# Kernel optimization log

Hardware: AMD Instinct MI355X
Metric: run time of the kernel (lower is better)

The kernel has to match this reference:

```python
import jax, jax.numpy as jnp
import numpy as np

B, S, H, DK = 2, 2048, 16, 64
D = H * DK  # d_model = 1024


def setup_inputs() -> dict:
    key = jax.random.key(0)
    ks = jax.random.split(key, 12)
    inp = {
        "queries": jax.random.normal(ks[0], (B, S, D), jnp.float32),
        "keys": jax.random.normal(ks[1], (B, S, D), jnp.float32),
        "values": jax.random.normal(ks[2], (B, S, D), jnp.float32),
        # additive 0/1 mask (1 = masked out), causal upper-triangular
        "mask": jnp.triu(jnp.ones((S, S), jnp.float32), k=1)[None, None, :, :],
        "W_q": jax.random.normal(ks[3], (D, D), jnp.float32) / np.sqrt(D),
        "b_q": jnp.zeros((D,), jnp.float32),
        "W_k": jax.random.normal(ks[4], (D, D), jnp.float32) / np.sqrt(D),
        "b_k": jnp.zeros((D,), jnp.float32),
        "W_v": jax.random.normal(ks[5], (D, D), jnp.float32) / np.sqrt(D),
        "b_v": jnp.zeros((D,), jnp.float32),
        "W_o": jax.random.normal(ks[6], (D, D), jnp.float32) / np.sqrt(D),
        "b_o": jnp.zeros((D,), jnp.float32),
    }
    return inp


def _split_heads(x):
    # (B, S, D) -> (B, H, S, DK)
    return x.reshape(x.shape[0], x.shape[1], H, DK).transpose(0, 2, 1, 3)


def reference(queries, keys, values, mask, W_q, b_q, W_k, b_k, W_v, b_v, W_o, b_o):
    q = _split_heads(queries @ W_q + b_q)  # (B, H, S, DK)
    k = _split_heads(keys @ W_k + b_k)
    v = _split_heads(values @ W_v + b_v)
    scale = 1.0 / jnp.sqrt(jnp.asarray(DK, q.dtype))
    scores = jnp.einsum("bhqd,bhkd->bhqk", q, k) * scale  # (B, H, S, S)
    scores = scores + (-1e9) * mask
    weights = jax.nn.softmax(scores, axis=-1)
    o = jnp.einsum("bhqk,bhkd->bhqd", weights, v)  # (B, H, S, DK)
    o = o.transpose(0, 2, 1, 3).reshape(queries.shape[0], queries.shape[1], D)
    return o @ W_o + b_o
```

## Files before the change

kernel.cpp:

```cpp
#include <hip/hip_runtime.h>
#include <hip/hip_bf16.h>
#include <stdint.h>

typedef unsigned short u16;
typedef __attribute__((ext_vector_type(4))) float f32x4;
typedef __attribute__((ext_vector_type(8))) short bf16x8;
typedef __attribute__((ext_vector_type(4))) short s16x4;

#define B_ 2
#define S_ 2048
#define H_ 16
#define D_ 1024
#define XELEMS (B_*S_*D_)
#define WELEMS (D_*D_)
#define QSCALE 0.18033688f

__device__ __forceinline__ u16 f2bf(float f) {
  union { float f; unsigned u; } v; v.f = f;
  unsigned r = v.u + 0x7fffu + ((v.u >> 16) & 1u);
  return (u16)(r >> 16);
}

__device__ __forceinline__ void async16(const void* g, void* l) {
  __builtin_amdgcn_global_load_lds(
      (const __attribute__((address_space(1))) unsigned int*)g,
      (__attribute__((address_space(3))) unsigned int*)l, 16, 0, 0);
}

#if __has_builtin(__builtin_amdgcn_exp2f)
#define EXP2(x) __builtin_amdgcn_exp2f(x)
#else
#define EXP2(x) exp2f(x)
#endif

__device__ __forceinline__ unsigned cvtpk(float a, float b) {
  unsigned r;
  asm("v_cvt_pk_bf16_f32 %0, %1, %2" : "=v"(r) : "v"(a), "v"(b));
  return r;
}

#if __has_builtin(__builtin_amdgcn_mfma_f32_16x16x16bf16_1k)
#define MFMA16(a, b, c) __builtin_amdgcn_mfma_f32_16x16x16bf16_1k(a, b, c, 0, 0, 0)
#else
__device__ __forceinline__ f32x4 mfma16_(s16x4 a, s16x4 b, f32x4 c) {
  asm("v_mfma_f32_16x16x16_bf16 %0, %1, %2, %0" : "+v"(c) : "v"(a), "v"(b));
  return c;
}
#define MFMA16(a, b, c) mfma16_(a, b, c)
#endif

__global__ __launch_bounds__(256) void prep_k(
    const float* __restrict__ q, const float* __restrict__ k,
    const float* __restrict__ v,
    const float* __restrict__ Wq, const float* __restrict__ Wk,
    const float* __restrict__ Wv, const float* __restrict__ Wo,
    u16* __restrict__ X, u16* __restrict__ WT) {
  const int bid = blockIdx.x;
  if (bid < 4096) {
    __shared__ float tile[32][33];
    const int z = bid >> 10, rem = bid & 1023;
    const float* W = (z == 0) ? Wq : (z == 1) ? Wk : (z == 2) ? Wv : Wo;
    u16* o = WT + z * WELEMS;
    const int r0 = (rem >> 5) << 5, c0 = (rem & 31) << 5;
    const int tx = threadIdx.x & 31, ty = threadIdx.x >> 5;
    #pragma unroll
    for (int rr = ty; rr < 32; rr += 8)
      tile[rr][tx] = W[(r0 + rr) * D_ + c0 + tx];
    __syncthreads();
    #pragma unroll
    for (int rr = ty; rr < 32; rr += 8)
      o[(c0 + rr) * D_ + r0 + tx] = f2bf(tile[tx][rr]);
  } else {
    const int cb = bid - 4096;
    const int ngrp = XELEMS / 8;
    const int total = 3 * ngrp;
    for (int i = cb * 256 + threadIdx.x; i < total; i += 1024 * 256) {
      int which = i / ngrp;
      int off = (i - which * ngrp) * 8;
      const float* src = (which == 0) ? q : (which == 1) ? k : v;
      float4 a = *(const float4*)(src + off);
      float4 b = *(const float4*)(src + off + 4);
      u16 rr[8] = {f2bf(a.x), f2bf(a.y), f2bf(a.z), f2bf(a.w),
                   f2bf(b.x), f2bf(b.y), f2bf(b.z), f2bf(b.w)};
      uint4 pk;
      pk.x = (unsigned)rr[0] | ((unsigned)rr[1] << 16);
      pk.y = (unsigned)rr[2] | ((unsigned)rr[3] << 16);
      pk.z = (unsigned)rr[4] | ((unsigned)rr[5] << 16);
      pk.w = (unsigned)rr[6] | ((unsigned)rr[7] << 16);
      *(uint4*)(X + which * XELEMS + off) = pk;
    }
  }
}

template <int MODE, int DBUF>
__device__ __forceinline__ void gemm_body(const u16* __restrict__ A,
                                          const u16* __restrict__ BT,
                                          const float* __restrict__ bias,
                                          void* __restrict__ outp,
                                          int bm, int bn, float scale) {
  constexpr int SMEM_BYTES = DBUF ? 65536 : ((MODE == 0 || MODE == 2) ? 34816 : 32768);
  __shared__ __align__(16) char smem[SMEM_BYTES];
  const int tid = threadIdx.x;
  const int w = tid >> 6, l = tid & 63;
  const int wr = w >> 1, wc = w & 1;
  const int g = l >> 4, r = l & 15;
  (void)w; (void)l;

  f32x4 acc[4][4];
  #pragma unroll
  for (int i = 0; i < 4; i++)
    #pragma unroll
    for (int j = 0; j < 4; j++) acc[i][j] = (f32x4){0.f, 0.f, 0.f, 0.f};

  int dst[4], aoff[4], boff[4];
  #pragma unroll
  for (int i = 0; i < 4; i++) {
    const int o = i * 4096 + tid * 16;
    dst[i] = o;
    const int row = o >> 7;
    const int cbyte = (o & 127) ^ ((row & 7) << 4);
    aoff[i] = (bm + row) * 1024 + (cbyte >> 1);
    boff[i] = (bn + row) * 1024 + (cbyte >> 1);
  }

  if (DBUF == 0) {
    char* Ab = smem;
    char* Bb = smem + 16384;
    for (int t = 0; t < 16; ++t) {
      const int k0 = t * 64;
      #pragma unroll
      for (int i = 0; i < 4; i++) async16(A + aoff[i] + k0, Ab + dst[i]);
      #pragma unroll
      for (int i = 0; i < 4; i++) async16(BT + boff[i] + k0, Bb + dst[i]);
      __syncthreads();
      bf16x8 af[2][4], bf[2][4];
      #pragma unroll
      for (int kk = 0; kk < 2; kk++)
        #pragma unroll
        for (int mi = 0; mi < 4; mi++) {
          const int rA = wr * 64 + mi * 16 + r;
          af[kk][mi] = *(const bf16x8*)(Ab +
              ((rA * 128 + kk * 64 + g * 16) ^ ((rA & 7) << 4)));
        }
      #pragma unroll
      for (int kk = 0; kk < 2; kk++)
        #pragma unroll
        for (int ni = 0; ni < 4; ni++) {
          const int rB = wc * 64 + ni * 16 + r;
          bf[kk][ni] = *(const bf16x8*)(Bb +
              ((rB * 128 + kk * 64 + g * 16) ^ ((rB & 7) << 4)));
        }
      #pragma unroll
      for (int kk = 0; kk < 2; kk++)
        #pragma unroll
        for (int mi = 0; mi < 4; mi++)
          #pragma unroll
          for (int ni = 0; ni < 4; ni++)
            acc[mi][ni] = __builtin_amdgcn_mfma_f32_16x16x32_bf16(
                af[kk][mi], bf[kk][ni], acc[mi][ni], 0, 0, 0);
      __syncthreads();
    }
  } else {
    #pragma unroll
    for (int i = 0; i < 4; i++) {
      async16(A + aoff[i], smem + dst[i]);
      async16(BT + boff[i], smem + 16384 + dst[i]);
    }
    for (int t = 0; t < 16; ++t) {
      const int buf = t & 1;
      const char* Ab = smem + buf * 32768;
      const char* Bb = Ab + 16384;
      if (t < 15) {
        const int k0 = (t + 1) * 64;
        char* An = smem + (buf ^ 1) * 32768;
        #pragma unroll
        for (int i = 0; i < 4; i++) {
          async16(A + aoff[i] + k0, An + dst[i]);
          async16(BT + boff[i] + k0, An + 16384 + dst[i]);
        }
        asm volatile("s_waitcnt vmcnt(8)" ::: "memory");
      } else {
        asm volatile("s_waitcnt vmcnt(0)" ::: "memory");
      }
      asm volatile("s_barrier" ::: "memory");

      bf16x8 af[2][4], bf[2][4];
      #pragma unroll
      for (int kk = 0; kk < 2; kk++)
        #pragma unroll
        for (int mi = 0; mi < 4; mi++) {
          const int rA = wr * 64 + mi * 16 + r;
          af[kk][mi] = *(const bf16x8*)(Ab +
              ((rA * 128 + kk * 64 + g * 16) ^ ((rA & 7) << 4)));
        }
      #pragma unroll
      for (int kk = 0; kk < 2; kk++)
        #pragma unroll
        for (int ni = 0; ni < 4; ni++) {
          const int rB = wc * 64 + ni * 16 + r;
          bf[kk][ni] = *(const bf16x8*)(Bb +
              ((rB * 128 + kk * 64 + g * 16) ^ ((rB & 7) << 4)));
        }
      __builtin_amdgcn_s_setprio(1);
      #pragma unroll
      for (int kk = 0; kk < 2; kk++)
        #pragma unroll
        for (int mi = 0; mi < 4; mi++)
          #pragma unroll
          for (int ni = 0; ni < 4; ni++)
            acc[mi][ni] = __builtin_amdgcn_mfma_f32_16x16x32_bf16(
                af[kk][mi], bf[kk][ni], acc[mi][ni], 0, 0, 0);
      __builtin_amdgcn_s_setprio(0);
      asm volatile("s_barrier" ::: "memory");
    }
  }

  const int col0 = bn + wc * 64;
  float bc[4];
  #pragma unroll
  for (int ni = 0; ni < 4; ni++) bc[ni] = bias[col0 + ni * 16 + r];

  if (MODE == 0) {
    u16* Ts = (u16*)smem;
    #pragma unroll
    for (int mi = 0; mi < 4; mi++) {
      #pragma unroll
      for (int ni = 0; ni < 4; ni++) {
        const int lcol = wc * 64 + ni * 16 + r;
        #pragma unroll
        for (int i = 0; i < 4; i++) {
          const int lrow = wr * 64 + mi * 16 + g * 4 + i;
          Ts[lrow * 136 + lcol] = f2bf((acc[mi][ni][i] + bc[ni]) * scale);
        }
      }
    }
    __syncthreads();
    u16* out = (u16*)outp;
    const int bb = bm >> 11;
    const int sbase = bm & 2047;
    #pragma unroll
    for (int j = 0; j < 8; j++) {
      const int c = j * 256 + tid;
      const int row = c >> 4, oct = c & 15;
      const int col = bn + oct * 8;
      const int h = col >> 6, dk = col & 63;
      bf16x8 vv = *(const bf16x8*)&Ts[row * 136 + oct * 8];
      *(bf16x8*)&out[(((size_t)((bb << 4) | h) * 2048 + sbase + row) << 6) + dk] = vv;
    }
  } else if (MODE == 2) {
    u16* Ts = (u16*)smem;
    #pragma unroll
    for (int mi = 0; mi < 4; mi++) {
      const int lrow = wr * 64 + mi * 16 + g * 4;
      #pragma unroll
      for (int ni = 0; ni < 4; ni++) {
        const int lcol = wc * 64 + ni * 16 + r;
        u16 p0 = f2bf(acc[mi][ni][0] + bc[ni]);
        u16 p1 = f2bf(acc[mi][ni][1] + bc[ni]);
        u16 p2 = f2bf(acc[mi][ni][2] + bc[ni]);
        u16 p3 = f2bf(acc[mi][ni][3] + bc[ni]);
        uint2 pk;
        pk.x = (unsigned)p0 | ((unsigned)p1 << 16);
        pk.y = (unsigned)p2 | ((unsigned)p3 << 16);
        *(uint2*)&Ts[lcol * 136 + lrow] = pk;
      }
    }
    __syncthreads();
    u16* out = (u16*)outp;
    const int bb = bm >> 11;
    const int sbase = bm & 2047;
    #pragma unroll
    for (int j = 0; j < 8; j++) {
      const int c = (tid >> 6) * 512 + j * 64 + (tid & 63);
      const int dk = c >> 4, sc = c & 15;
      const int col = bn + dk;
      const int h = col >> 6, dkk = col & 63;
      bf16x8 vv = *(const bf16x8*)&Ts[dk * 136 + sc * 8];
      *(bf16x8*)&out[(((size_t)(((bb << 4) | h) * 64 + dkk)) << 11) +
                     sbase + sc * 8] = vv;
    }
  } else {
    float* out = (float*)outp;
    #pragma unroll
    for (int mi = 0; mi < 4; mi++) {
      const int row = bm + wr * 64 + mi * 16 + g * 4;
      #pragma unroll
      for (int ni = 0; ni < 4; ni++) {
        const int col = col0 + ni * 16 + r;
        #pragma unroll
        for (int i = 0; i < 4; i++)
          out[(row + i) * 1024 + col] = acc[mi][ni][i] + bc[ni];
      }
    }
  }
}

__global__ __launch_bounds__(256) void gemm_qkv_k(
    const u16* __restrict__ X, const u16* __restrict__ WT,
    const float* __restrict__ bq, const float* __restrict__ bk,
    const float* __restrict__ bv, u16* __restrict__ QKV) {
  const int z = blockIdx.z;
  const float* bias = (z == 0) ? bq : (z == 1) ? bk : bv;
  if (z == 2)
    gemm_body<2, 0>(X + z * XELEMS, WT + z * WELEMS, bias, QKV + z * XELEMS,
                    blockIdx.x * 128, blockIdx.y * 128, 1.0f);
  else
    gemm_body<0, 0>(X + z * XELEMS, WT + z * WELEMS, bias, QKV + z * XELEMS,
                    blockIdx.x * 128, blockIdx.y * 128,
                    (z == 0) ? QSCALE : 1.0f);
}

__global__ __launch_bounds__(256) void gemm_o_k(
    const u16* __restrict__ O, const u16* __restrict__ WOT,
    const float* __restrict__ bo, float* __restrict__ out) {
  gemm_body<1, 1>(O, WOT, bo, out, blockIdx.x * 128, blockIdx.y * 128, 1.0f);
}

__global__ __launch_bounds__(512) void attn_k(
    const u16* __restrict__ Qh, const u16* __restrict__ Kh,
    const u16* __restrict__ VTh, u16* __restrict__ O) {
  __shared__ __align__(16) char ldsK[3][8192];
  __shared__ __align__(16) char ldsV[3][8192];

  const int bh = blockIdx.y;
  const int pj = blockIdx.x;
  const int tid = threadIdx.x;
  const int w = tid >> 6, l = tid & 63;
  const int grp = w >> 2, wg = w & 3;
  const int g = l >> 4, r = l & 15;
  const int b = bh >> 4, h = bh & 15;
  const int pjx = b ? (15 - pj) : pj;

  const u16* Qp = Qh + bh * (S_ * 64);
  const char* Kp = (const char*)(Kh + bh * (S_ * 64));
  const char* Vp = (const char*)(VTh + bh * (64 * S_));

  const int o = w * 1024 + l * 16;
  const int kdst = o;
  const int ksrc = o ^ (((o >> 7) & 7) << 4);
  const int vd = o >> 7, vcb = o & 127;
  const int vfix = vd * (S_ * 2) + (vcb ^ ((vd & 7) << 4));

  const int qt = grp ? (31 - pjx) : pjx;
  const int q0w = qt * 64 + wg * 16;
  const int my_nt = qt + 1;
  const int nt_max = 32 - pjx;
  const int qloc = wg * 16 + r;

  bf16x8 qf[2];
  #pragma unroll
  for (int dh = 0; dh < 2; dh++)
    qf[dh] = *(const bf16x8*)(Qp + (q0w + r) * 64 + dh * 32 + g * 8);
  asm volatile("s_waitcnt vmcnt(0)" ::: "memory");

  f32x4 accT[4];
  #pragma unroll
  for (int dn = 0; dn < 4; dn++) accT[dn] = (f32x4){0.f, 0.f, 0.f, 0.f};
  float mrun = -1e30f, lsum = 0.f;

  async16(Kp + ksrc, &ldsK[0][0] + kdst);
  async16(Vp + vfix, &ldsV[0][0] + kdst);
  async16(Kp + 8192 + ksrc, &ldsK[1][0] + kdst);
  async16(Vp + 128 + vfix, &ldsV[1][0] + kdst);

  int cur = 0, pre = 2;
  for (int t = 0; t < nt_max; ++t) {
    if (t + 2 < nt_max) {
      async16(Kp + (t + 2) * 8192 + ksrc, &ldsK[pre][0] + kdst);
      async16(Vp + (t + 2) * 128 + vfix, &ldsV[pre][0] + kdst);
      asm volatile("s_waitcnt vmcnt(4)" ::: "memory");
    } else if (t + 1 < nt_max) {
      asm volatile("s_waitcnt vmcnt(2)" ::: "memory");
    } else {
      asm volatile("s_waitcnt vmcnt(0)" ::: "memory");
    }
    asm volatile("s_barrier" ::: "memory");

    if (t < my_nt) {
      const char* Kb = &ldsK[cur][0];
      f32x4 sc[4];
      #pragma unroll
      for (int ct = 0; ct < 4; ct++) {
        const int row = ct * 16 + r;
        const int sw = (row & 7) << 4;
        bf16x8 k0 = *(const bf16x8*)(Kb + ((row * 128 + g * 16) ^ sw));
        bf16x8 k1 = *(const bf16x8*)(Kb + ((row * 128 + 64 + g * 16) ^ sw));
        f32x4 z = (f32x4){0.f, 0.f, 0.f, 0.f};
        z = __builtin_amdgcn_mfma_f32_16x16x32_bf16(k0, qf[0], z, 0, 0, 0);
        sc[ct] = __builtin_amdgcn_mfma_f32_16x16x32_bf16(k1, qf[1], z, 0, 0, 0);
      }

      if (t == my_nt - 1) {
        #pragma unroll
        for (int ct = 0; ct < 4; ct++)
          #pragma unroll
          for (int i = 0; i < 4; i++)
            if (ct * 16 + g * 4 + i > qloc) sc[ct][i] = -1e9f;
      }

      float a0 = fmaxf(fmaxf(sc[0][0], sc[0][1]), sc[0][2]);
      float a1 = fmaxf(fmaxf(sc[0][3], sc[1][0]), sc[1][1]);
      float a2 = fmaxf(fmaxf(sc[1][2], sc[1][3]), sc[2][0]);
      float a3 = fmaxf(fmaxf(sc[2][1], sc[2][2]), sc[2][3]);
      float a4 = fmaxf(fmaxf(sc[3][0], sc[3][1]), sc[3][2]);
      float pmax = fmaxf(fmaxf(fmaxf(a0, a1), fmaxf(a2, a3)),
                         fmaxf(a4, sc[3][3]));

      if (!__all(pmax - mrun <= 11.0f)) {
        float pm = fmaxf(pmax, __shfl_xor(pmax, 16, 64));
        pm = fmaxf(pm, __shfl_xor(pm, 32, 64));
        const float mnew = fmaxf(mrun, pm);
        const float corr = EXP2(mrun - mnew);
        mrun = mnew;
        #pragma unroll
        for (int dn = 0; dn < 4; dn++)
          #pragma unroll
          for (int i = 0; i < 4; i++) accT[dn][i] *= corr;
        lsum *= corr;
      }

      float ps = 0.f;
      #pragma unroll
      for (int ct = 0; ct < 4; ct++)
        #pragma unroll
        for (int i = 0; i < 4; i++) {
          const float p = EXP2(sc[ct][i] - mrun);
          sc[ct][i] = p;
          ps += p;
        }
      lsum += ps;

      s16x4 pb[4];
      #pragma unroll
      for (int ct = 0; ct < 4; ct++) {
        union { uint2 u; s16x4 s; } cvt;
        cvt.u.x = cvtpk(sc[ct][0], sc[ct][1]);
        cvt.u.y = cvtpk(sc[ct][2], sc[ct][3]);
        pb[ct] = cvt.s;
      }

      const char* Vb = &ldsV[cur][0];
      __builtin_amdgcn_s_setprio(1);
      #pragma unroll
      for (int dn = 0; dn < 4; dn++) {
        const int vrow = dn * 16 + r;
        const int rowb = vrow * 128;
        const int sw = (vrow & 7) << 4;
        #pragma unroll
        for (int ct = 0; ct < 4; ct++) {
          s16x4 va = *(const s16x4*)(Vb + (rowb + ((ct * 32 + g * 8) ^ sw)));
          accT[dn] = MFMA16(va, pb[ct], accT[dn]);
        }
      }
      __builtin_amdgcn_s_setprio(0);
    }
    asm volatile("s_barrier" ::: "memory");
    cur = (cur == 2) ? 0 : cur + 1;
    pre = (pre == 2) ? 0 : pre + 1;
  }

  float lrow = lsum + __shfl_xor(lsum, 16, 64);
  lrow = lrow + __shfl_xor(lrow, 32, 64);
  const float inv = 1.0f / lrow;
  const int qrow = q0w + r;
  #pragma unroll
  for (int dn = 0; dn < 4; dn++) {
    u16 o0 = f2bf(accT[dn][0] * inv), o1 = f2bf(accT[dn][1] * inv);
    u16 o2 = f2bf(accT[dn][2] * inv), o3 = f2bf(accT[dn][3] * inv);
    uint2 pk;
    pk.x = (unsigned)o0 | ((unsigned)o1 << 16);
    pk.y = (unsigned)o2 | ((unsigned)o3 << 16);
    *(uint2*)(O + ((size_t)(b * 2048 + qrow)) * 1024 + h * 64 + dn * 16 + g * 4) = pk;
  }
}

extern "C" void kernel_launch(void* const* d_in, const int* in_sizes, int n_in,
                              void* d_out, int out_size, void* d_ws, size_t ws_size,
                              hipStream_t stream) {
  const float* q  = (const float*)d_in[0];
  const float* k  = (const float*)d_in[1];
  const float* v  = (const float*)d_in[2];
  const float* Wq = (const float*)d_in[4];
  const float* bq = (const float*)d_in[5];
  const float* Wk = (const float*)d_in[6];
  const float* bk = (const float*)d_in[7];
  const float* Wv = (const float*)d_in[8];
  const float* bv = (const float*)d_in[9];
  const float* Wo = (const float*)d_in[10];
  const float* bo = (const float*)d_in[11];

  char* ws = (char*)d_ws;
  const size_t MB = 1u << 20;
  u16* X   = (u16*)(ws);
  u16* WT  = (u16*)(ws + 24 * MB);
  u16* QKV = (u16*)(ws + 32 * MB);
  u16* O   = (u16*)(ws);

  hipLaunchKernelGGL(prep_k, dim3(5120), dim3(256), 0, stream,
                     q, k, v, Wq, Wk, Wv, Wo, X, WT);
  hipLaunchKernelGGL(gemm_qkv_k, dim3(32, 8, 3), dim3(256), 0, stream,
                     X, WT, bq, bk, bv, QKV);
  hipLaunchKernelGGL(attn_k, dim3(16, 32), dim3(512), 0, stream,
                     QKV, QKV + XELEMS, QKV + 2 * XELEMS, O);
  hipLaunchKernelGGL(gemm_o_k, dim3(32, 8), dim3(256), 0, stream,
                     O, WT + 3 * WELEMS, bo, (float*)d_out);
}
```

Before: 122.1 us.

## Give each attention block four query tiles with two q-subtiles per wave

Each attention workgroup now handles four 64-row query tiles (pj, 31-pj, 15-pj, 16+pj), with each wave owning 32 query rows as two 16-row subtiles. Every K/V fragment read from LDS therefore feeds two MFMAs, and each staged K/V tile is shared by more query rows. The grid shrinks from 16x32 to 8x32 blocks. In exchange, register pressure roughly doubles for accumulators and scores, there are fewer blocks to fill the GPU, and the per-batch load-balancing flip is dropped.

Measured after the change: 131.9 us. 8.0% more time.

```diff
diff --git a/kernel.cpp b/kernel.cpp
--- a/kernel.cpp
+++ b/kernel.cpp
@@ -326,10 +326,11 @@
   const int pj = blockIdx.x;
   const int tid = threadIdx.x;
   const int w = tid >> 6, l = tid & 63;
-  const int grp = w >> 2, wg = w & 3;
   const int g = l >> 4, r = l & 15;
   const int b = bh >> 4, h = bh & 15;
-  const int pjx = b ? (15 - pj) : pj;
+  const int tsel = w >> 1, wg = w & 1;
+  const int qt = (tsel == 0) ? pj : (tsel == 1) ? (31 - pj)
+               : (tsel == 2) ? (15 - pj) : (16 + pj);
 
   const u16* Qp = Qh + bh * (S_ * 64);
   const char* Kp = (const char*)(Kh + bh * (S_ * 64));
@@ -341,22 +342,24 @@
   const int vd = o >> 7, vcb = o & 127;
   const int vfix = vd * (S_ * 2) + (vcb ^ ((vd & 7) << 4));
 
-  const int qt = grp ? (31 - pjx) : pjx;
-  const int q0w = qt * 64 + wg * 16;
+  const int q0w = qt * 64 + wg * 32;
   const int my_nt = qt + 1;
-  const int nt_max = 32 - pjx;
-  const int qloc = wg * 16 + r;
-
-  bf16x8 qf[2];
+  const int nt_max = 32 - pj;
+
+  bf16x8 qf[2][2];
   #pragma unroll
-  for (int dh = 0; dh < 2; dh++)
-    qf[dh] = *(const bf16x8*)(Qp + (q0w + r) * 64 + dh * 32 + g * 8);
+  for (int qq = 0; qq < 2; qq++)
+    #pragma unroll
+    for (int dh = 0; dh < 2; dh++)
+      qf[qq][dh] = *(const bf16x8*)(Qp + (q0w + qq * 16 + r) * 64 + dh * 32 + g * 8);
   asm volatile("s_waitcnt vmcnt(0)" ::: "memory");
 
-  f32x4 accT[4];
+  f32x4 accT[2][4];
   #pragma unroll
-  for (int dn = 0; dn < 4; dn++) accT[dn] = (f32x4){0.f, 0.f, 0.f, 0.f};
-  float mrun = -1e30f, lsum = 0.f;
+  for (int qq = 0; qq < 2; qq++)
+    #pragma unroll
+    for (int dn = 0; dn < 4; dn++) accT[qq][dn] = (f32x4){0.f, 0.f, 0.f, 0.f};
+  float mrun[2] = {-1e30f, -1e30f}, lsum[2] = {0.f, 0.f};
 
   async16(Kp + ksrc, &ldsK[0][0] + kdst);
   async16(Vp + vfix, &ldsV[0][0] + kdst);
@@ -378,65 +381,75 @@
 
     if (t < my_nt) {
       const char* Kb = &ldsK[cur][0];
-      f32x4 sc[4];
+      f32x4 sc[2][4];
       #pragma unroll
       for (int ct = 0; ct < 4; ct++) {
         const int row = ct * 16 + r;
         const int sw = (row & 7) << 4;
         bf16x8 k0 = *(const bf16x8*)(Kb + ((row * 128 + g * 16) ^ sw));
         bf16x8 k1 = *(const bf16x8*)(Kb + ((row * 128 + 64 + g * 16) ^ sw));
-        f32x4 z = (f32x4){0.f, 0.f, 0.f, 0.f};
-        z = __builtin_amdgcn_mfma_f32_16x16x32_bf16(k0, qf[0], z, 0, 0, 0);
-        sc[ct] = __builtin_amdgcn_mfma_f32_16x16x32_bf16(k1, qf[1], z, 0, 0, 0);
+        #pragma unroll
+        for (int qq = 0; qq < 2; qq++) {
+          f32x4 z = (f32x4){0.f, 0.f, 0.f, 0.f};
+          z = __builtin_amdgcn_mfma_f32_16x16x32_bf16(k0, qf[qq][0], z, 0, 0, 0);
+          sc[qq][ct] = __builtin_amdgcn_mfma_f32_16x16x32_bf16(k1, qf[qq][1], z, 0, 0, 0);
+        }
       }
 
       if (t == my_nt - 1) {
+        #pragma unroll
+        for (int qq = 0; qq < 2; qq++) {
+          const int qloc = wg * 32 + qq * 16 + r;
+          #pragma unroll
+          for (int ct = 0; ct < 4; ct++)
+            #pragma unroll
+            for (int i = 0; i < 4; i++)
+              if (ct * 16 + g * 4 + i > qloc) sc[qq][ct][i] = -1e9f;
+        }
+      }
+
+      s16x4 pb[2][4];
+      #pragma unroll
+      for (int qq = 0; qq < 2; qq++) {
+        float a0 = fmaxf(fmaxf(sc[qq][0][0], sc[qq][0][1]), sc[qq][0][2]);
+        float a1 = fmaxf(fmaxf(sc[qq][0][3], sc[qq][1][0]), sc[qq][1][1]);
+        float a2 = fmaxf(fmaxf(sc[qq][1][2], sc[qq][1][3]), sc[qq][2][0]);
+        float a3 = fmaxf(fmaxf(sc[qq][2][1], sc[qq][2][2]), sc[qq][2][3]);
+        float a4 = fmaxf(fmaxf(sc[qq][3][0], sc[qq][3][1]), sc[qq][3][2]);
+        float pmax = fmaxf(fmaxf(fmaxf(a0, a1), fmaxf(a2, a3)),
+                           fmaxf(a4, sc[qq][3][3]));
+
+        if (!__all(pmax - mrun[qq] <= 11.0f)) {
+          float pm = fmaxf(pmax, __shfl_xor(pmax, 16, 64));
+          pm = fmaxf(pm, __shfl_xor(pm, 32, 64));
+          const float mnew = fmaxf(mrun[qq], pm);
+          const float corr = EXP2(mrun[qq] - mnew);
+          mrun[qq] = mnew;
+          #pragma unroll
+          for (int dn = 0; dn < 4; dn++)
+            #pragma unroll
+            for (int i = 0; i < 4; i++) accT[qq][dn][i] *= corr;
+          lsum[qq] *= corr;
+        }
+
+        float ps = 0.f;
         #pragma unroll
         for (int ct = 0; ct < 4; ct++)
           #pragma unroll
-          for (int i = 0; i < 4; i++)
-            if (ct * 16 + g * 4 + i > qloc) sc[ct][i] = -1e9f;
-      }
-
-      float a0 = fmaxf(fmaxf(sc[0][0], sc[0][1]), sc[0][2]);
-      float a1 = fmaxf(fmaxf(sc[0][3], sc[1][0]), sc[1][1]);
-      float a2 = fmaxf(fmaxf(sc[1][2], sc[1][3]), sc[2][0]);
-      float a3 = fmaxf(fmaxf(sc[2][1], sc[2][2]), sc[2][3]);
-      float a4 = fmaxf(fmaxf(sc[3][0], sc[3][1]), sc[3][2]);
-      float pmax = fmaxf(fmaxf(fmaxf(a0, a1), fmaxf(a2, a3)),
-                         fmaxf(a4, sc[3][3]));
-
-      if (!__all(pmax - mrun <= 11.0f)) {
-        float pm = fmaxf(pmax, __shfl_xor(pmax, 16, 64));
-        pm = fmaxf(pm, __shfl_xor(pm, 32, 64));
-        const float mnew = fmaxf(mrun, pm);
-        const float corr = EXP2(mrun - mnew);
-        mrun = mnew;
-        #pragma unroll
-        for (int dn = 0; dn < 4; dn++)
-          #pragma unroll
-          for (int i = 0; i < 4; i++) accT[dn][i] *= corr;
-        lsum *= corr;
-      }
-
-      float ps = 0.f;
-      #pragma unroll
-      for (int ct = 0; ct < 4; ct++)
-        #pragma unroll
-        for (int i = 0; i < 4; i++) {
-          const float p = EXP2(sc[ct][i] - mrun);
-          sc[ct][i] = p;
-          ps += p;
-        }
-      lsum += ps;
-
-      s16x4 pb[4];
-      #pragma unroll
-      for (int ct = 0; ct < 4; ct++) {
-        union { uint2 u; s16x4 s; } cvt;
-        cvt.u.x = cvtpk(sc[ct][0], sc[ct][1]);
-        cvt.u.y = cvtpk(sc[ct][2], sc[ct][3]);
-        pb[ct] = cvt.s;
+          for (int i = 0; i < 4; i++) {
+            const float p = EXP2(sc[qq][ct][i] - mrun[qq]);
+            sc[qq][ct][i] = p;
+            ps += p;
+          }
+        lsum[qq] += ps;
+
+        #pragma unroll
+        for (int ct = 0; ct < 4; ct++) {
+          union { uint2 u; s16x4 s; } cvt;
+          cvt.u.x = cvtpk(sc[qq][ct][0], sc[qq][ct][1]);
+          cvt.u.y = cvtpk(sc[qq][ct][2], sc[qq][ct][3]);
+          pb[qq][ct] = cvt.s;
+        }
       }
 
       const char* Vb = &ldsV[cur][0];
@@ -449,7 +462,8 @@
         #pragma unroll
         for (int ct = 0; ct < 4; ct++) {
           s16x4 va = *(const s16x4*)(Vb + (rowb + ((ct * 32 + g * 8) ^ sw)));
-          accT[dn] = MFMA16(va, pb[ct], accT[dn]);
+          accT[0][dn] = MFMA16(va, pb[0][ct], accT[0][dn]);
+          accT[1][dn] = MFMA16(va, pb[1][ct], accT[1][dn]);
         }
       }
       __builtin_amdgcn_s_setprio(0);
@@ -459,18 +473,21 @@
     pre = (pre == 2) ? 0 : pre + 1;
   }
 
-  float lrow = lsum + __shfl_xor(lsum, 16, 64);
-  lrow = lrow + __shfl_xor(lrow, 32, 64);
-  const float inv = 1.0f / lrow;
-  const int qrow = q0w + r;
   #pragma unroll
-  for (int dn = 0; dn < 4; dn++) {
-    u16 o0 = f2bf(accT[dn][0] * inv), o1 = f2bf(accT[dn][1] * inv);
-    u16 o2 = f2bf(accT[dn][2] * inv), o3 = f2bf(accT[dn][3] * inv);
-    uint2 pk;
-    pk.x = (unsigned)o0 | ((unsigned)o1 << 16);
-    pk.y = (unsigned)o2 | ((unsigned)o3 << 16);
-    *(uint2*)(O + ((size_t)(b * 2048 + qrow)) * 1024 + h * 64 + dn * 16 + g * 4) = pk;
+  for (int qq = 0; qq < 2; qq++) {
+    float lrow = lsum[qq] + __shfl_xor(lsum[qq], 16, 64);
+    lrow = lrow + __shfl_xor(lrow, 32, 64);
+    const float inv = 1.0f / lrow;
+    const int qrow = q0w + qq * 16 + r;
+    #pragma unroll
+    for (int dn = 0; dn < 4; dn++) {
+      u16 o0 = f2bf(accT[qq][dn][0] * inv), o1 = f2bf(accT[qq][dn][1] * inv);
+      u16 o2 = f2bf(accT[qq][dn][2] * inv), o3 = f2bf(accT[qq][dn][3] * inv);
+      uint2 pk;
+      pk.x = (unsigned)o0 | ((unsigned)o1 << 16);
+      pk.y = (unsigned)o2 | ((unsigned)o3 << 16);
+      *(uint2*)(O + ((size_t)(b * 2048 + qrow)) * 1024 + h * 64 + dn * 16 + g * 4) = pk;
+    }
   }
 }
 
@@ -500,7 +517,7 @@
                      q, k, v, Wq, Wk, Wv, Wo, X, WT);
   hipLaunchKernelGGL(gemm_qkv_k, dim3(32, 8, 3), dim3(256), 0, stream,
                      X, WT, bq, bk, bv, QKV);
-  hipLaunchKernelGGL(attn_k, dim3(16, 32), dim3(512), 0, stream,
+  hipLaunchKernelGGL(attn_k, dim3(8, 32), dim3(512), 0, stream,
                      QKV, QKV + XELEMS, QKV + 2 * XELEMS, O);
   hipLaunchKernelGGL(gemm_o_k, dim3(32, 8), dim3(256), 0, stream,
                      O, WT + 3 * WELEMS, bo, (float*)d_out);
```
